# Kernel tuning notes

Hardware: AMD Instinct MI355X
Metric: run time of the kernel (lower is better)

Reference implementation:

```python
import jax, jax.numpy as jnp
import numpy as np

DIM = 1024
NUM_HEADS = 16
HEAD_DIM = DIM // NUM_HEADS
SCALE = HEAD_DIM ** -0.5


def setup_inputs() -> dict:
    key = jax.random.key(0)
    k1, k2, k3 = jax.random.split(key, 3)
    x = jax.random.normal(k1, (2, 2048, DIM), dtype=jnp.float32)
    # nn.Linear weights: stored as [out, in]; y = x @ W.T
    w_qkv = jax.random.normal(k2, (3 * DIM, DIM), dtype=jnp.float32) * (DIM ** -0.5)
    w_proj = jax.random.normal(k3, (DIM, DIM), dtype=jnp.float32) * (DIM ** -0.5)
    return {"x": x, "w_qkv": w_qkv, "w_proj": w_proj}


def reference(x, w_qkv, w_proj):
    B, L, D = x.shape
    qkv = jnp.einsum("bld,ed->ble", x, w_qkv)  # [B, L, 3*D]
    qkv = qkv.reshape(B, L, 3, NUM_HEADS, HEAD_DIM).transpose(2, 0, 3, 1, 4)
    q, k, v = qkv[0], qkv[1], qkv[2]  # each [B, H, L, hd]
    attn = jnp.einsum("bhqd,bhkd->bhqk", q, k) * SCALE
    attn = jax.nn.softmax(attn, axis=-1)
    out = jnp.einsum("bhqk,bhkd->bhqd", attn, v)  # [B, H, L, hd]
    out = out.transpose(0, 2, 1, 3).reshape(B, L, D)
    return jnp.einsum("bld,ed->ble", out, w_proj)
```

## Files before the change

### kernel.cpp

```cpp
#include <hip/hip_runtime.h>
#include <math.h>
#include <stdint.h>

#define B_ 2
#define L_ 2048
#define D_ 1024
#define H_ 16
#define HD_ 64
#define SCALE_ 0.125f

typedef __attribute__((ext_vector_type(8))) short short8;
typedef __attribute__((ext_vector_type(4))) short short4v;
typedef __attribute__((ext_vector_type(4))) float float4v;

__device__ __forceinline__ short f2bf(float f) {
    union { float f; unsigned u; } x; x.f = f;
    unsigned r = x.u + 0x7fffu + ((x.u >> 16) & 1u);
    return (short)(r >> 16);
}

__device__ __forceinline__ void gl_lds16(const void* g, void* l) {
    __builtin_amdgcn_global_load_lds(
        (const __attribute__((address_space(1))) unsigned int*)g,
        (__attribute__((address_space(3))) unsigned int*)l, 16, 0, 0);
}

__global__ __launch_bounds__(256) void cvt_bf16(const float* __restrict__ in,
                                                short* __restrict__ out, int n4) {
    int i = blockIdx.x * 256 + threadIdx.x;
    if (i >= n4) return;
    float4 v = ((const float4*)in)[i];
    short4v o;
    o.x = f2bf(v.x); o.y = f2bf(v.y); o.z = f2bf(v.z); o.w = f2bf(v.w);
    ((short4v*)out)[i] = o;
}

__global__ __launch_bounds__(256) void gemm_qkv_bf16(const short* __restrict__ A,
                                                     const short* __restrict__ Bm,
                                                     short* __restrict__ Qb,
                                                     short* __restrict__ Kb,
                                                     short* __restrict__ Vb) {
    __shared__ short As[128 * 32];
    __shared__ short Bs[128 * 32];
    const int tid = threadIdx.x;
    const int w = tid >> 6, l = tid & 63;
    const int lm = l & 15, q = l >> 4;
    const int m0 = blockIdx.y * 128, n0 = blockIdx.x * 128;
    const int wm = w >> 1, wn = w & 1;

    float4v acc[4][4];
#pragma unroll
    for (int mt = 0; mt < 4; ++mt)
#pragma unroll
        for (int nt = 0; nt < 4; ++nt) acc[mt][nt] = (float4v){0.f, 0.f, 0.f, 0.f};

    for (int k0 = 0; k0 < 1024; k0 += 32) {
        __syncthreads();
#pragma unroll
        for (int t = 0; t < 2; ++t) {
            int idx8 = w * 128 + t * 64 + l;
            int row = idx8 >> 2, c8 = idx8 & 3;
            gl_lds16(A  + (size_t)(m0 + row) * 1024 + k0 + c8 * 8, (char*)As + w * 2048 + t * 1024);
            gl_lds16(Bm + (size_t)(n0 + row) * 1024 + k0 + c8 * 8, (char*)Bs + w * 2048 + t * 1024);
        }
        __syncthreads();
        short8 af[4], bfr[4];
#pragma unroll
        for (int mt = 0; mt < 4; ++mt)
            af[mt] = *(const short8*)(As + (wm * 64 + mt * 16 + lm) * 32 + q * 8);
#pragma unroll
        for (int nt = 0; nt < 4; ++nt)
            bfr[nt] = *(const short8*)(Bs + (wn * 64 + nt * 16 + lm) * 32 + q * 8);
#pragma unroll
        for (int mt = 0; mt < 4; ++mt)
#pragma unroll
            for (int nt = 0; nt < 4; ++nt)
                acc[mt][nt] = __builtin_amdgcn_mfma_f32_16x16x32_bf16(af[mt], bfr[nt], acc[mt][nt], 0, 0, 0);
    }

    const int which = n0 >> 10;
    if (which < 2) {
        short* dst = (which == 0) ? Qb : Kb;
        const float sc = (which == 0) ? SCALE_ : 1.0f;
#pragma unroll
        for (int mt = 0; mt < 4; ++mt) {
#pragma unroll
            for (int nt = 0; nt < 4; ++nt) {
                const int n = n0 + wn * 64 + nt * 16 + lm;
                const int h = (n & 1023) >> 6, d = n & 63;
#pragma unroll
                for (int r = 0; r < 4; ++r) {
                    const int m = m0 + wm * 64 + mt * 16 + q * 4 + r;
                    const int b = m >> 11, ll = m & 2047;
                    dst[(((size_t)b * H_ + h) * L_ + ll) * HD_ + d] = f2bf(acc[mt][nt][r] * sc);
                }
            }
        }
    } else {
#pragma unroll
        for (int mt = 0; mt < 4; ++mt) {
            const int m = m0 + wm * 64 + mt * 16 + q * 4;
            const int b = m >> 11, ll = m & 2047;
#pragma unroll
            for (int nt = 0; nt < 4; ++nt) {
                const int n = n0 + wn * 64 + nt * 16 + lm;
                const int h = (n & 1023) >> 6, d = n & 63;
                short4v pk;
                pk.x = f2bf(acc[mt][nt][0]); pk.y = f2bf(acc[mt][nt][1]);
                pk.z = f2bf(acc[mt][nt][2]); pk.w = f2bf(acc[mt][nt][3]);
                *(short4v*)(Vb + (((size_t)b * H_ + h) * HD_ + d) * L_ + ll) = pk;
            }
        }
    }
}

__global__ __launch_bounds__(256) void attn_mfma(const short* __restrict__ Qb,
                                                 const short* __restrict__ Kb,
                                                 const short* __restrict__ Vtg,
                                                 short* __restrict__ Ob) {
    __shared__ short Ql[128 * 64];
    __shared__ short Kl[64 * 64];
    __shared__ short Vt[64 * 64];
    __shared__ short Pt[128 * 72];

    const int tid = threadIdx.x;
    const int w = tid >> 6, l = tid & 63;
    const int lm = l & 15, q = l >> 4;
    const int qt = blockIdx.x, bh = blockIdx.y;

    const short* Qg = Qb  + ((size_t)bh * L_ + qt * 128) * HD_;
    const short* Kg = Kb  + (size_t)bh * L_ * HD_;
    const short* Vg = Vtg + (size_t)bh * HD_ * L_;

#pragma unroll
    for (int t = 0; t < 4; ++t) {
        int idx = tid + 256 * t;
        int row = idx >> 3, c = idx & 7;
        short8 v = *(const short8*)(Qg + row * 64 + c * 8);
        *(short8*)(Ql + row * 64 + ((c ^ (row & 7)) * 8)) = v;
    }

    const int srow = tid >> 3;
    const int sc   = tid & 7;
    const int koff0 = srow * 64 + ((sc ^ (srow & 7)) * 8);
    const int koff1 = koff0 + 32 * 64;

    short8 kreg0 = *(const short8*)(Kg + (size_t)srow * 64 + sc * 8);
    short8 kreg1 = *(const short8*)(Kg + (size_t)(srow + 32) * 64 + sc * 8);
    short8 vreg0 = *(const short8*)(Vg + (size_t)srow * L_ + sc * 8);
    short8 vreg1 = *(const short8*)(Vg + (size_t)(srow + 32) * L_ + sc * 8);

    __syncthreads();

    short8 qf[2][2];
#pragma unroll
    for (int nq = 0; nq < 2; ++nq)
#pragma unroll
        for (int kh = 0; kh < 2; ++kh) {
            int row = w * 32 + nq * 16 + lm;
            int ch = kh * 4 + q;
            qf[nq][kh] = *(const short8*)(Ql + row * 64 + ((ch ^ (row & 7)) * 8));
        }

    float4v o[4][2];
#pragma unroll
    for (int mt = 0; mt < 4; ++mt)
#pragma unroll
        for (int nq = 0; nq < 2; ++nq) o[mt][nq] = (float4v){0.f, 0.f, 0.f, 0.f};
    float lsum[2] = {0.f, 0.f};

    const int prow = w * 32 + lm;

    for (int t = 0; t < 32; ++t) {
        __syncthreads();
        *(short8*)(Kl + koff0) = kreg0;
        *(short8*)(Kl + koff1) = kreg1;
        *(short8*)(Vt + koff0) = vreg0;
        *(short8*)(Vt + koff1) = vreg1;
        __syncthreads();
        if (t < 31) {
            kreg0 = *(const short8*)(Kg + (size_t)((t + 1) * 64 + srow) * 64 + sc * 8);
            kreg1 = *(const short8*)(Kg + (size_t)((t + 1) * 64 + srow + 32) * 64 + sc * 8);
            vreg0 = *(const short8*)(Vg + (size_t)srow * L_ + (t + 1) * 64 + sc * 8);
            vreg1 = *(const short8*)(Vg + (size_t)(srow + 32) * L_ + (t + 1) * 64 + sc * 8);
        }

        float4v st[4][2];
#pragma unroll
        for (int nt = 0; nt < 4; ++nt) {
            const int arow = nt * 16 + lm;
            short8 a0 = *(const short8*)(Kl + arow * 64 + ((q ^ (arow & 7)) * 8));
            short8 a1 = *(const short8*)(Kl + arow * 64 + (((4 + q) ^ (arow & 7)) * 8));
#pragma unroll
            for (int nq = 0; nq < 2; ++nq) {
                float4v z = (float4v){0.f, 0.f, 0.f, 0.f};
                z = __builtin_amdgcn_mfma_f32_16x16x32_bf16(a0, qf[nq][0], z, 0, 0, 0);
                z = __builtin_amdgcn_mfma_f32_16x16x32_bf16(a1, qf[nq][1], z, 0, 0, 0);
                st[nt][nq] = z;
            }
        }

#pragma unroll
        for (int nt = 0; nt < 4; ++nt)
#pragma unroll
            for (int nq = 0; nq < 2; ++nq) {
                const float e0 = __expf(st[nt][nq][0]);
                const float e1 = __expf(st[nt][nq][1]);
                const float e2 = __expf(st[nt][nq][2]);
                const float e3 = __expf(st[nt][nq][3]);
                lsum[nq] += (e0 + e1) + (e2 + e3);
                short4v pk;
                pk.x = f2bf(e0); pk.y = f2bf(e1); pk.z = f2bf(e2); pk.w = f2bf(e3);
                *(short4v*)(Pt + (prow + nq * 16) * 72 + nt * 16 + q * 4) = pk;
            }

#pragma unroll
        for (int kh = 0; kh < 2; ++kh) {
            short8 pb[2];
#pragma unroll
            for (int nq = 0; nq < 2; ++nq)
                pb[nq] = *(const short8*)(Pt + (prow + nq * 16) * 72 + kh * 32 + q * 8);
#pragma unroll
            for (int mt = 0; mt < 4; ++mt) {
                const int arow = mt * 16 + lm;
                short8 va = *(const short8*)(Vt + arow * 64 + (((kh * 4 + q) ^ (arow & 7)) * 8));
#pragma unroll
                for (int nq = 0; nq < 2; ++nq)
                    o[mt][nq] = __builtin_amdgcn_mfma_f32_16x16x32_bf16(va, pb[nq], o[mt][nq], 0, 0, 0);
            }
        }
    }

    float inv[2];
#pragma unroll
    for (int nq = 0; nq < 2; ++nq) {
        float s = lsum[nq];
        s += __shfl_xor(s, 16);
        s += __shfl_xor(s, 32);
        inv[nq] = 1.f / s;
    }
    short* OgBase = Ob + ((size_t)bh * L_ + qt * 128) * HD_;
#pragma unroll
    for (int nq = 0; nq < 2; ++nq) {
        const int qrow = w * 32 + nq * 16 + lm;
#pragma unroll
        for (int mt = 0; mt < 4; ++mt) {
            short4v pk;
            pk.x = f2bf(o[mt][nq][0] * inv[nq]);
            pk.y = f2bf(o[mt][nq][1] * inv[nq]);
            pk.z = f2bf(o[mt][nq][2] * inv[nq]);
            pk.w = f2bf(o[mt][nq][3] * inv[nq]);
            *(short4v*)(OgBase + (size_t)qrow * 64 + mt * 16 + q * 4) = pk;
        }
    }
}

__global__ __launch_bounds__(256) void gemm_proj_bf16(const short* __restrict__ Ob,
                                                      const short* __restrict__ Wp,
                                                      float* __restrict__ out) {
    __shared__ short As[64 * 32];
    __shared__ short Bs[128 * 32];
    const int tid = threadIdx.x;
    const int w = tid >> 6, l = tid & 63;
    const int lm = l & 15, q = l >> 4;
    const int m0 = blockIdx.y * 64, n0 = blockIdx.x * 128;
    const int wm = w & 1, wn = w >> 1;
    const int b = m0 >> 11, l0 = m0 & 2047;

    float4v acc[2][4];
#pragma unroll
    for (int mt = 0; mt < 2; ++mt)
#pragma unroll
        for (int nt = 0; nt < 4; ++nt) acc[mt][nt] = (float4v){0.f, 0.f, 0.f, 0.f};

    for (int k0 = 0; k0 < 1024; k0 += 32) {
        __syncthreads();
        {
            int idx8 = w * 64 + l;
            int row = idx8 >> 2, c8 = idx8 & 3;
            int h = k0 >> 6, d = (k0 & 32) + c8 * 8;
            gl_lds16(Ob + (((size_t)b * H_ + h) * L_ + l0 + row) * HD_ + d, (char*)As + w * 1024);
        }
#pragma unroll
        for (int t = 0; t < 2; ++t) {
            int idx8 = w * 128 + t * 64 + l;
            int row = idx8 >> 2, c8 = idx8 & 3;
            gl_lds16(Wp + (size_t)(n0 + row) * 1024 + k0 + c8 * 8, (char*)Bs + w * 2048 + t * 1024);
        }
        __syncthreads();
        short8 af[2], bfr[4];
#pragma unroll
        for (int mt = 0; mt < 2; ++mt)
            af[mt] = *(const short8*)(As + (wm * 32 + mt * 16 + lm) * 32 + q * 8);
#pragma unroll
        for (int nt = 0; nt < 4; ++nt)
            bfr[nt] = *(const short8*)(Bs + (wn * 64 + nt * 16 + lm) * 32 + q * 8);
#pragma unroll
        for (int mt = 0; mt < 2; ++mt)
#pragma unroll
            for (int nt = 0; nt < 4; ++nt)
                acc[mt][nt] = __builtin_amdgcn_mfma_f32_16x16x32_bf16(af[mt], bfr[nt], acc[mt][nt], 0, 0, 0);
    }

#pragma unroll
    for (int mt = 0; mt < 2; ++mt)
#pragma unroll
        for (int nt = 0; nt < 4; ++nt)
#pragma unroll
            for (int r = 0; r < 4; ++r) {
                const int m = m0 + wm * 32 + mt * 16 + q * 4 + r;
                const int n = n0 + wn * 64 + nt * 16 + lm;
                out[(size_t)m * 1024 + n] = acc[mt][nt][r];
            }
}

extern "C" void kernel_launch(void* const* d_in, const int* in_sizes, int n_in,
                              void* d_out, int out_size, void* d_ws, size_t ws_size,
                              hipStream_t stream) {
    (void)in_sizes; (void)n_in; (void)out_size; (void)ws_size;
    const float* x      = (const float*)d_in[0];
    const float* w_qkv  = (const float*)d_in[1];
    const float* w_proj = (const float*)d_in[2];

    char* ws = (char*)d_ws;
    short* xb     = (short*)(ws);
    short* wqkvb  = (short*)(ws + (8u  << 20));
    short* wprojb = (short*)(ws + (14u << 20));
    short* Qb     = (short*)(ws + (16u << 20));
    short* Kb     = (short*)(ws + (24u << 20));
    short* Vb     = (short*)(ws + (32u << 20));
    short* Ob     = xb;

    cvt_bf16<<<4096, 256, 0, stream>>>(x,      xb,     1048576);
    cvt_bf16<<<3072, 256, 0, stream>>>(w_qkv,  wqkvb,   786432);
    cvt_bf16<<<1024, 256, 0, stream>>>(w_proj, wprojb,  262144);
    gemm_qkv_bf16 <<<dim3(24, 32), 256, 0, stream>>>(xb, wqkvb, Qb, Kb, Vb);
    attn_mfma     <<<dim3(16, 32), 256, 0, stream>>>(Qb, Kb, Vb, Ob);
    gemm_proj_bf16<<<dim3(8, 64),  256, 0, stream>>>(Ob, wprojb, (float*)d_out);
}
```

Before: 206.2 us.

## Double-buffer K/V tiles, stage Q/K epilogue through LDS, use exp2

The attention kernel now double-buffers the K/V shared-memory tiles, which removes one of the two barriers per iteration and prefetches two tiles ahead. The QKV GEMM epilogue for Q and K now goes through LDS so that global stores are coalesced 16-byte writes instead of scattered 2-byte ones. The log2(e) factor is folded into the Q scale so the kernel can call a native exp2 in place of __expf, and the swizzled LDS offsets are precomputed outside the loop. The cost is more LDS and registers per block, which may lower occupancy.

New measurement: 201.0 us. -2.5%, faster.

```diff
diff --git a/kernel.cpp b/kernel.cpp
--- a/kernel.cpp
+++ b/kernel.cpp
@@ -7,11 +7,20 @@
 #define D_ 1024
 #define H_ 16
 #define HD_ 64
-#define SCALE_ 0.125f
+#define QSCALE_ 0.1803368801f
 
 typedef __attribute__((ext_vector_type(8))) short short8;
 typedef __attribute__((ext_vector_type(4))) short short4v;
 typedef __attribute__((ext_vector_type(4))) float float4v;
+
+#if defined(__has_builtin)
+#if __has_builtin(__builtin_amdgcn_exp2f)
+#define EXP2F(x) __builtin_amdgcn_exp2f(x)
+#endif
+#endif
+#ifndef EXP2F
+#define EXP2F(x) exp2f(x)
+#endif
 
 __device__ __forceinline__ short f2bf(float f) {
     union { float f; unsigned u; } x; x.f = f;
@@ -40,8 +49,9 @@
                                                      short* __restrict__ Qb,
                                                      short* __restrict__ Kb,
                                                      short* __restrict__ Vb) {
-    __shared__ short As[128 * 32];
-    __shared__ short Bs[128 * 32];
+    __shared__ short smem[8192];
+    short* As = smem;
+    short* Bs = smem + 4096;
     const int tid = threadIdx.x;
     const int w = tid >> 6, l = tid & 63;
     const int lm = l & 15, q = l >> 4;
@@ -81,19 +91,31 @@
     const int which = n0 >> 10;
     if (which < 2) {
         short* dst = (which == 0) ? Qb : Kb;
-        const float sc = (which == 0) ? SCALE_ : 1.0f;
-#pragma unroll
-        for (int mt = 0; mt < 4; ++mt) {
-#pragma unroll
-            for (int nt = 0; nt < 4; ++nt) {
-                const int n = n0 + wn * 64 + nt * 16 + lm;
-                const int h = (n & 1023) >> 6, d = n & 63;
-#pragma unroll
-                for (int r = 0; r < 4; ++r) {
-                    const int m = m0 + wm * 64 + mt * 16 + q * 4 + r;
-                    const int b = m >> 11, ll = m & 2047;
-                    dst[(((size_t)b * H_ + h) * L_ + ll) * HD_ + d] = f2bf(acc[mt][nt][r] * sc);
-                }
+        const float sc = (which == 0) ? QSCALE_ : 1.0f;
+#pragma unroll
+        for (int half = 0; half < 2; ++half) {
+            __syncthreads();
+            if (wm == half) {
+#pragma unroll
+                for (int mt = 0; mt < 4; ++mt)
+#pragma unroll
+                    for (int nt = 0; nt < 4; ++nt)
+#pragma unroll
+                        for (int r = 0; r < 4; ++r)
+                            smem[(mt * 16 + q * 4 + r) * 128 + wn * 64 + nt * 16 + lm] =
+                                f2bf(acc[mt][nt][r] * sc);
+            }
+            __syncthreads();
+#pragma unroll
+            for (int j = 0; j < 4; ++j) {
+                const int x = tid + 256 * j;
+                const int row = x >> 4, c = x & 15;
+                short8 v = *(const short8*)(smem + row * 128 + c * 8);
+                const int m = m0 + half * 64 + row;
+                const int b = m >> 11, ll = m & 2047;
+                const int n = n0 + c * 8;
+                const int hh = (n & 1023) >> 6, d = n & 63;
+                *(short8*)(dst + (((size_t)b * H_ + hh) * L_ + ll) * HD_ + d) = v;
             }
         }
     } else {
@@ -119,8 +141,7 @@
                                                  const short* __restrict__ Vtg,
                                                  short* __restrict__ Ob) {
     __shared__ short Ql[128 * 64];
-    __shared__ short Kl[64 * 64];
-    __shared__ short Vt[64 * 64];
+    __shared__ short KV[4 * 4096];
     __shared__ short Pt[128 * 72];
 
     const int tid = threadIdx.x;
@@ -145,10 +166,20 @@
     const int koff0 = srow * 64 + ((sc ^ (srow & 7)) * 8);
     const int koff1 = koff0 + 32 * 64;
 
-    short8 kreg0 = *(const short8*)(Kg + (size_t)srow * 64 + sc * 8);
-    short8 kreg1 = *(const short8*)(Kg + (size_t)(srow + 32) * 64 + sc * 8);
-    short8 vreg0 = *(const short8*)(Vg + (size_t)srow * L_ + sc * 8);
-    short8 vreg1 = *(const short8*)(Vg + (size_t)(srow + 32) * L_ + sc * 8);
+    {
+        short8 ka = *(const short8*)(Kg + (size_t)srow * 64 + sc * 8);
+        short8 kb = *(const short8*)(Kg + (size_t)(srow + 32) * 64 + sc * 8);
+        short8 va = *(const short8*)(Vg + (size_t)srow * L_ + sc * 8);
+        short8 vb = *(const short8*)(Vg + (size_t)(srow + 32) * L_ + sc * 8);
+        *(short8*)(KV + koff0) = ka;
+        *(short8*)(KV + koff1) = kb;
+        *(short8*)(KV + 4096 + koff0) = va;
+        *(short8*)(KV + 4096 + koff1) = vb;
+    }
+    short8 kra = *(const short8*)(Kg + (size_t)(64 + srow) * 64 + sc * 8);
+    short8 krb = *(const short8*)(Kg + (size_t)(64 + srow + 32) * 64 + sc * 8);
+    short8 vra = *(const short8*)(Vg + (size_t)srow * L_ + 64 + sc * 8);
+    short8 vrb = *(const short8*)(Vg + (size_t)(srow + 32) * L_ + 64 + sc * 8);
 
     __syncthreads();
 
@@ -162,6 +193,17 @@
             qf[nq][kh] = *(const short8*)(Ql + row * 64 + ((ch ^ (row & 7)) * 8));
         }
 
+    int offA0[4], offA1[4], offV[2][4];
+#pragma unroll
+    for (int nt = 0; nt < 4; ++nt) {
+        const int arow = nt * 16 + lm;
+        offA0[nt] = arow * 64 + ((q ^ (arow & 7)) * 8);
+        offA1[nt] = arow * 64 + (((4 + q) ^ (arow & 7)) * 8);
+#pragma unroll
+        for (int kh = 0; kh < 2; ++kh)
+            offV[kh][nt] = arow * 64 + (((kh * 4 + q) ^ (arow & 7)) * 8);
+    }
+
     float4v o[4][2];
 #pragma unroll
     for (int mt = 0; mt < 4; ++mt)
@@ -171,26 +213,34 @@
 
     const int prow = w * 32 + lm;
 
+#pragma unroll 2
     for (int t = 0; t < 32; ++t) {
-        __syncthreads();
-        *(short8*)(Kl + koff0) = kreg0;
-        *(short8*)(Kl + koff1) = kreg1;
-        *(short8*)(Vt + koff0) = vreg0;
-        *(short8*)(Vt + koff1) = vreg1;
-        __syncthreads();
+        const int cur = t & 1;
+        short* Kl = KV + cur * 8192;
+        short* Vt = Kl + 4096;
+        short* Kn = KV + (1 - cur) * 8192;
+        short* Vn = Kn + 4096;
+
+        __syncthreads();
+
         if (t < 31) {
-            kreg0 = *(const short8*)(Kg + (size_t)((t + 1) * 64 + srow) * 64 + sc * 8);
-            kreg1 = *(const short8*)(Kg + (size_t)((t + 1) * 64 + srow + 32) * 64 + sc * 8);
-            vreg0 = *(const short8*)(Vg + (size_t)srow * L_ + (t + 1) * 64 + sc * 8);
-            vreg1 = *(const short8*)(Vg + (size_t)(srow + 32) * L_ + (t + 1) * 64 + sc * 8);
+            *(short8*)(Kn + koff0) = kra;
+            *(short8*)(Kn + koff1) = krb;
+            *(short8*)(Vn + koff0) = vra;
+            *(short8*)(Vn + koff1) = vrb;
+        }
+        if (t < 30) {
+            kra = *(const short8*)(Kg + (size_t)((t + 2) * 64 + srow) * 64 + sc * 8);
+            krb = *(const short8*)(Kg + (size_t)((t + 2) * 64 + srow + 32) * 64 + sc * 8);
+            vra = *(const short8*)(Vg + (size_t)srow * L_ + (t + 2) * 64 + sc * 8);
+            vrb = *(const short8*)(Vg + (size_t)(srow + 32) * L_ + (t + 2) * 64 + sc * 8);
         }
 
         float4v st[4][2];
 #pragma unroll
         for (int nt = 0; nt < 4; ++nt) {
-            const int arow = nt * 16 + lm;
-            short8 a0 = *(const short8*)(Kl + arow * 64 + ((q ^ (arow & 7)) * 8));
-            short8 a1 = *(const short8*)(Kl + arow * 64 + (((4 + q) ^ (arow & 7)) * 8));
+            short8 a0 = *(const short8*)(Kl + offA0[nt]);
+            short8 a1 = *(const short8*)(Kl + offA1[nt]);
 #pragma unroll
             for (int nq = 0; nq < 2; ++nq) {
                 float4v z = (float4v){0.f, 0.f, 0.f, 0.f};
@@ -204,10 +254,10 @@
         for (int nt = 0; nt < 4; ++nt)
 #pragma unroll
             for (int nq = 0; nq < 2; ++nq) {
-                const float e0 = __expf(st[nt][nq][0]);
-                const float e1 = __expf(st[nt][nq][1]);
-                const float e2 = __expf(st[nt][nq][2]);
-                const float e3 = __expf(st[nt][nq][3]);
+                const float e0 = EXP2F(st[nt][nq][0]);
+                const float e1 = EXP2F(st[nt][nq][1]);
+                const float e2 = EXP2F(st[nt][nq][2]);
+                const float e3 = EXP2F(st[nt][nq][3]);
                 lsum[nq] += (e0 + e1) + (e2 + e3);
                 short4v pk;
                 pk.x = f2bf(e0); pk.y = f2bf(e1); pk.z = f2bf(e2); pk.w = f2bf(e3);
@@ -222,8 +272,7 @@
                 pb[nq] = *(const short8*)(Pt + (prow + nq * 16) * 72 + kh * 32 + q * 8);
 #pragma unroll
             for (int mt = 0; mt < 4; ++mt) {
-                const int arow = mt * 16 + lm;
-                short8 va = *(const short8*)(Vt + arow * 64 + (((kh * 4 + q) ^ (arow & 7)) * 8));
+                short8 va = *(const short8*)(Vt + offV[kh][mt]);
 #pragma unroll
                 for (int nq = 0; nq < 2; ++nq)
                     o[mt][nq] = __builtin_amdgcn_mfma_f32_16x16x32_bf16(va, pb[nq], o[mt][nq], 0, 0, 0);
```
